# Kernel tuning notes

Measured on AMD Instinct MI355X. Metric: run time of the kernel, lower is better.

Reference implementation:

```python
import jax, jax.numpy as jnp
import numpy as np

H = 512          # size_half
K = 16           # n_segments
B = 8192         # batch
WIDTH = 1.0 / K  # spline bin width


def setup_inputs() -> dict:
    key = jax.random.key(0)
    ks = jax.random.split(key, 4)
    v_in = jax.random.uniform(ks[0], (B, 2 * H), dtype=jnp.float32)  # config in [0,1]
    log_density = jax.random.normal(ks[1], (B, 1), dtype=jnp.float32)
    W1 = jax.random.normal(ks[2], (H, H), dtype=jnp.float32) * (1.0 / np.sqrt(H))
    b1 = jnp.zeros((H,), dtype=jnp.float32)
    W2 = jax.random.normal(ks[3], (H, H * K), dtype=jnp.float32) * (1.0 / np.sqrt(H))
    b2 = jnp.zeros((H * K,), dtype=jnp.float32)
    return {"v_in": v_in, "log_density": log_density, "W1": W1, "b1": b1, "W2": W2, "b2": b2}


def reference(v_in, log_density, W1, b1, W2, b2):
    # even_sites=True: passive = first half, active = second half
    v_passive = v_in[:, :H]           # [B, H]
    v_active = v_in[:, H:]            # [B, H]

    # FullyConnectedNeuralNetwork: hidden layer + final layer, tanh activation on both
    h = jnp.tanh((v_passive - 0.5) @ W1 + b1)          # [B, H]
    net = jnp.tanh(h @ W2 + b2).reshape(-1, H, K)      # [B, H, K]
    p = jax.nn.softmax(net, axis=2)                    # bin probability masses P_k

    # y-coordinates of knots: CDF of the bin masses, with leading zero
    knots_y = jnp.concatenate(
        [jnp.zeros((p.shape[0], H, 1), p.dtype), jnp.cumsum(p, axis=2)], axis=2
    )                                                  # [B, H, K+1]

    # searchsorted on uniform knots linspace(0,1,K+1), then -1, clamped
    knots_x = jnp.linspace(0.0, 1.0, K + 1, dtype=v_in.dtype)
    k = jnp.clip(jnp.searchsorted(knots_x, v_active, side="left") - 1, 0, K - 1)  # [B, H]

    p_k = jnp.take_along_axis(p, k[..., None], axis=2)[..., 0]        # [B, H]
    y_lo = jnp.take_along_axis(knots_y, k[..., None], axis=2)[..., 0]  # [B, H]

    alpha = (v_active - k.astype(v_in.dtype) * WIDTH) / WIDTH          # [B, H]
    v_out_active = y_lo + alpha * p_k

    v_out = jnp.concatenate([v_passive, v_out_active], axis=1)         # [B, 2H]
    log_density_out = log_density - jnp.sum(jnp.log(p_k), axis=1, keepdims=True)  # [B, 1]
    return v_out, log_density_out
```

## Files before the change

kernel.cpp:

```cpp
#include <hip/hip_runtime.h>
#include <hip/hip_bf16.h>

#define HH   512
#define BB   8192
#define WIDTH (1.0f/16.0f)

typedef __attribute__((ext_vector_type(8))) short  short8;
typedef __attribute__((ext_vector_type(4))) float  floatx4;

typedef const __attribute__((address_space(1))) void* gptr_t;
typedef __attribute__((address_space(3))) void*       lptr_t;

__device__ __forceinline__ void gload_lds16(const void* g, void* l) {
    __builtin_amdgcn_global_load_lds((gptr_t)g, (lptr_t)l, 16, 0, 0);
}

__device__ __forceinline__ float tanh_fast(float x) {
    float e = __expf(2.0f * x);
    return 1.0f - 2.0f * __builtin_amdgcn_rcpf(e + 1.0f);
}

__global__ void prep_small(const float* __restrict__ vin, const float* __restrict__ W1,
                           const float* __restrict__ ld,
                           float* __restrict__ vout, float* __restrict__ ldout,
                           __hip_bfloat16* __restrict__ Abf,
                           __hip_bfloat16* __restrict__ W1T) {
    __shared__ __align__(16) float tile[32 * 36];
    int bid = blockIdx.x, tid = threadIdx.x;
    if (bid < 256) {
        int c0 = (bid & 15) * 32, r0 = (bid >> 4) * 32;
        int y  = tid >> 3;
        int x0 = (tid & 7) * 4;
        float4 v = *(const float4*)(W1 + (size_t)(r0 + y) * 512 + c0 + x0);
        *(float4*)(tile + y * 36 + x0) = v;
        __syncthreads();
        int n  = tid >> 3;
        int k4 = (tid & 7) * 4;
        union { __hip_bfloat16 h[4]; uint2 u; } o;
        o.h[0] = __float2bfloat16(tile[(k4 + 0) * 36 + n]);
        o.h[1] = __float2bfloat16(tile[(k4 + 1) * 36 + n]);
        o.h[2] = __float2bfloat16(tile[(k4 + 2) * 36 + n]);
        o.h[3] = __float2bfloat16(tile[(k4 + 3) * 36 + n]);
        *(uint2*)(W1T + (size_t)(c0 + n) * 512 + r0 + k4) = o.u;
    } else {
        int b = bid - 256;
        int i = b * 256 + tid;
        int r = i >> 6, c = i & 63;
        const float4* src = (const float4*)(vin + (size_t)r * 1024 + c * 8);
        float4 f0 = src[0], f1 = src[1];
        float4* dst = (float4*)(vout + (size_t)r * 1024 + c * 8);
        dst[0] = f0; dst[1] = f1;
        union { __hip_bfloat16 h[8]; uint4 v; } u;
        u.h[0] = __float2bfloat16(f0.x - 0.5f); u.h[1] = __float2bfloat16(f0.y - 0.5f);
        u.h[2] = __float2bfloat16(f0.z - 0.5f); u.h[3] = __float2bfloat16(f0.w - 0.5f);
        u.h[4] = __float2bfloat16(f1.x - 0.5f); u.h[5] = __float2bfloat16(f1.y - 0.5f);
        u.h[6] = __float2bfloat16(f1.z - 0.5f); u.h[7] = __float2bfloat16(f1.w - 0.5f);
        *(uint4*)(Abf + (size_t)r * 512 + c * 8) = u.v;
        if (tid < 4) { int row = b * 4 + tid; ldout[row] = ld[row]; }
    }
}

__global__ __launch_bounds__(256, 4) void mega1_kernel(
        const __hip_bfloat16* __restrict__ Abf,
        const __hip_bfloat16* __restrict__ W1T,
        const float* __restrict__ b1,
        __hip_bfloat16* __restrict__ hM,
        const float* __restrict__ W2,
        __hip_bfloat16* __restrict__ W2T) {
    __shared__ __align__(16) char smem[32768];
    int bid = blockIdx.x, tid = threadIdx.x;
    if (bid >= 256) {
        float* tile = (float*)smem;
        int b = bid - 256;
        int c0 = (b & 255) * 32, r0 = (b >> 8) * 32;
        int y  = tid >> 3;
        int x0 = (tid & 7) * 4;
        float4 v = *(const float4*)(W2 + (size_t)(r0 + y) * 8192 + c0 + x0);
        *(float4*)(tile + y * 36 + x0) = v;
        __syncthreads();
        int n  = tid >> 3;
        int k4 = (tid & 7) * 4;
        union { __hip_bfloat16 h[4]; uint2 u; } o;
        o.h[0] = __float2bfloat16(tile[(k4 + 0) * 36 + n]);
        o.h[1] = __float2bfloat16(tile[(k4 + 1) * 36 + n]);
        o.h[2] = __float2bfloat16(tile[(k4 + 2) * 36 + n]);
        o.h[3] = __float2bfloat16(tile[(k4 + 3) * 36 + n]);
        *(uint2*)(W2T + (size_t)(c0 + n) * 512 + r0 + k4) = o.u;
        return;
    }
    short* ldsA = (short*)smem;
    short* ldsB = (short*)(smem + 16384);
    int lane = tid & 63;
    int wv = tid >> 6, wr = wv >> 1, wc = wv & 1;
    int q = lane >> 4, cx = lane & 15;
    int srow = tid >> 3;
    int skw  = ((tid & 7) ^ (srow & 7)) * 8;
    int rowBase = (bid >> 2) * 128;
    int colBase = (bid & 3) * 128;
    floatx4 acc[4][4] = {};

    for (int k0 = 0; k0 < HH; k0 += 64) {
        #pragma unroll
        for (int j = 0; j < 4; ++j) {
            int row = j * 32 + srow;
            unsigned loff = __builtin_amdgcn_readfirstlane((unsigned)((j * 256 + (tid & 192)) * 16));
            gload_lds16(Abf + (size_t)(rowBase + row) * HH + k0 + skw, (char*)ldsA + loff);
            gload_lds16(W1T + (size_t)(colBase + row) * HH + k0 + skw, (char*)ldsB + loff);
        }
        __syncthreads();
        #pragma unroll
        for (int s = 0; s < 2; ++s) {
            short8 a[4], b[4];
            #pragma unroll
            for (int mt = 0; mt < 4; ++mt)
                a[mt] = *(const short8*)(ldsA + (wr * 64 + mt * 16 + cx) * 64
                                              + (((s * 4 + q) ^ (cx & 7)) << 3));
            #pragma unroll
            for (int nt = 0; nt < 4; ++nt)
                b[nt] = *(const short8*)(ldsB + (wc * 64 + nt * 16 + cx) * 64
                                              + (((s * 4 + q) ^ (cx & 7)) << 3));
            #pragma unroll
            for (int mt = 0; mt < 4; ++mt)
                #pragma unroll
                for (int nt = 0; nt < 4; ++nt)
                    acc[mt][nt] = __builtin_amdgcn_mfma_f32_16x16x32_bf16(a[mt], b[nt], acc[mt][nt], 0, 0, 0);
        }
        __syncthreads();
    }

    float b1v[4];
    #pragma unroll
    for (int nt = 0; nt < 4; ++nt) b1v[nt] = b1[colBase + wc * 64 + nt * 16 + cx];
    #pragma unroll
    for (int mt = 0; mt < 4; ++mt)
        #pragma unroll
        for (int nt = 0; nt < 4; ++nt) {
            int col = colBase + wc * 64 + nt * 16 + cx;
            #pragma unroll
            for (int r = 0; r < 4; ++r) {
                int row = rowBase + wr * 64 + mt * 16 + q * 4 + r;
                hM[(size_t)row * HH + col] = __float2bfloat16(tanh_fast(acc[mt][nt][r] + b1v[nt]));
            }
        }
}

__global__ __launch_bounds__(256, 4) void gemm2_kernel(
        const __hip_bfloat16* __restrict__ hM,
        const __hip_bfloat16* __restrict__ W2T,
        const float* __restrict__ b2,
        const float* __restrict__ vin,
        float* __restrict__ vout,
        float* __restrict__ ldout) {
    __shared__ __align__(16) char smem[32768];
    short* ldsA = (short*)smem;
    short* ldsB = (short*)(smem + 16384);
    float* ldsE = (float*)smem;
    int tid = threadIdx.x;
    int lane = tid & 63;
    int wv = tid >> 6, wr = wv >> 1, wc = wv & 1;
    int q = lane >> 4, cx = lane & 15;
    int srow = tid >> 3;
    int skw  = ((tid & 7) ^ (srow & 7)) * 8;
    int bid = blockIdx.x;
    int xcd = bid & 7, w = bid >> 3;
    int by  = xcd * 8 + (w & 7);
    int bx  = w >> 3;
    int rowBase = by * 128;
    int colBase = bx * 128;
    floatx4 acc[4][4] = {};

    for (int k0 = 0; k0 < HH; k0 += 64) {
        #pragma unroll
        for (int j = 0; j < 4; ++j) {
            int row = j * 32 + srow;
            unsigned loff = __builtin_amdgcn_readfirstlane((unsigned)((j * 256 + (tid & 192)) * 16));
            gload_lds16(hM  + (size_t)(rowBase + row) * HH + k0 + skw, (char*)ldsA + loff);
            gload_lds16(W2T + (size_t)(colBase + row) * HH + k0 + skw, (char*)ldsB + loff);
        }
        __syncthreads();
        #pragma unroll
        for (int s = 0; s < 2; ++s) {
            short8 a[4], b[4];
            #pragma unroll
            for (int mt = 0; mt < 4; ++mt)
                a[mt] = *(const short8*)(ldsA + (wr * 64 + mt * 16 + cx) * 64
                                              + (((s * 4 + q) ^ (cx & 7)) << 3));
            #pragma unroll
            for (int nt = 0; nt < 4; ++nt)
                b[nt] = *(const short8*)(ldsB + (wc * 64 + nt * 16 + cx) * 64
                                              + (((s * 4 + q) ^ (cx & 7)) << 3));
            #pragma unroll
            for (int mt = 0; mt < 4; ++mt)
                #pragma unroll
                for (int nt = 0; nt < 4; ++nt)
                    acc[mt][nt] = __builtin_amdgcn_mfma_f32_16x16x32_bf16(a[mt], b[nt], acc[mt][nt], 0, 0, 0);
        }
        __syncthreads();
    }

    float b2v[4];
    #pragma unroll
    for (int nt = 0; nt < 4; ++nt) b2v[nt] = b2[colBase + wc * 64 + nt * 16 + cx];

    float* myTile = ldsE + wv * (16 * 76);
    int rowL  = lane & 15;
    int gL    = lane >> 4;
    int gAbs  = bx * 8 + wc * 4 + gL;

    #pragma unroll
    for (int mt = 0; mt < 4; ++mt) {
        #pragma unroll
        for (int nt = 0; nt < 4; ++nt)
            #pragma unroll
            for (int r = 0; r < 4; ++r)
                myTile[(q * 4 + r) * 76 + nt * 16 + cx] = acc[mt][nt][r] + b2v[nt];

        floatx4 x0 = *(const floatx4*)(myTile + rowL * 76 + gL * 16);
        floatx4 x1 = *(const floatx4*)(myTile + rowL * 76 + gL * 16 + 4);
        floatx4 x2 = *(const floatx4*)(myTile + rowL * 76 + gL * 16 + 8);
        floatx4 x3 = *(const floatx4*)(myTile + rowL * 76 + gL * 16 + 12);
        float xs[16] = { x0[0],x0[1],x0[2],x0[3], x1[0],x1[1],x1[2],x1[3],
                         x2[0],x2[1],x2[2],x2[3], x3[0],x3[1],x3[2],x3[3] };

        int row = rowBase + wr * 64 + mt * 16 + rowL;
        float v = vin[(size_t)row * 1024 + 512 + gAbs];
        int k = (int)ceilf(v * 16.0f) - 1;
        k = min(15, max(0, k));

        float s = 0.0f, csum = 0.0f, ek = 0.0f;
        #pragma unroll
        for (int j = 0; j < 16; ++j) {
            float e2 = __expf(2.0f * xs[j]);
            float t  = 1.0f - 2.0f * __builtin_amdgcn_rcpf(e2 + 1.0f);
            float e  = __expf(t);
            csum += (j < k)  ? e : 0.0f;
            ek    = (j == k) ? e : ek;
            s += e;
        }
        float rs = __builtin_amdgcn_rcpf(s);
        float pk  = ek * rs;
        float ylo = csum * rs;
        float alpha = (v - (float)k * WIDTH) * 16.0f;
        vout[(size_t)row * 1024 + 512 + gAbs] = ylo + alpha * pk;

        float logp = __logf(pk);
        logp += __shfl_xor(logp, 16, 64);
        logp += __shfl_xor(logp, 32, 64);
        if (lane < 16) atomicAdd(ldout + row, -logp);
    }
}

extern "C" void kernel_launch(void* const* d_in, const int* in_sizes, int n_in,
                              void* d_out, int out_size, void* d_ws, size_t ws_size,
                              hipStream_t stream) {
    const float* vin = (const float*)d_in[0];
    const float* ld  = (const float*)d_in[1];
    const float* W1  = (const float*)d_in[2];
    const float* b1  = (const float*)d_in[3];
    const float* W2  = (const float*)d_in[4];
    const float* b2  = (const float*)d_in[5];
    float* vout  = (float*)d_out;
    float* ldout = vout + (size_t)BB * 1024;

    char* ws = (char*)d_ws;
    __hip_bfloat16* Abf = (__hip_bfloat16*)(ws);
    __hip_bfloat16* W1T = (__hip_bfloat16*)(ws + 8388608);
    __hip_bfloat16* W2T = (__hip_bfloat16*)(ws + 8912896);
    __hip_bfloat16* hM  = (__hip_bfloat16*)(ws + 17301504);

    prep_small<<<2304, 256, 0, stream>>>(vin, W1, ld, vout, ldout, Abf, W1T);
    mega1_kernel<<<4352, 256, 0, stream>>>(Abf, W1T, b1, hM, W2, W2T);
    gemm2_kernel<<<4096, 256, 0, stream>>>(hM, W2T, b2, vin, vout, ldout);
}
```

Baseline: 197.0 us.

## Fuse input/W1 bf16 conversion into GEMM1 and drop the prep kernel

```diff
diff --git a/kernel.cpp b/kernel.cpp
--- a/kernel.cpp
+++ b/kernel.cpp
@@ -20,55 +20,29 @@
     return 1.0f - 2.0f * __builtin_amdgcn_rcpf(e + 1.0f);
 }
 
-__global__ void prep_small(const float* __restrict__ vin, const float* __restrict__ W1,
-                           const float* __restrict__ ld,
-                           float* __restrict__ vout, float* __restrict__ ldout,
-                           __hip_bfloat16* __restrict__ Abf,
-                           __hip_bfloat16* __restrict__ W1T) {
-    __shared__ __align__(16) float tile[32 * 36];
+__global__ __launch_bounds__(256, 4) void mega_kernel(
+        const float* __restrict__ vin,
+        const float* __restrict__ W1,
+        const float* __restrict__ b1,
+        __hip_bfloat16* __restrict__ hM,
+        const float* __restrict__ W2,
+        __hip_bfloat16* __restrict__ W2T,
+        const float* __restrict__ ld,
+        float* __restrict__ vout, float* __restrict__ ldout) {
+    __shared__ __align__(16) char smem[32768];
     int bid = blockIdx.x, tid = threadIdx.x;
-    if (bid < 256) {
-        int c0 = (bid & 15) * 32, r0 = (bid >> 4) * 32;
-        int y  = tid >> 3;
-        int x0 = (tid & 7) * 4;
-        float4 v = *(const float4*)(W1 + (size_t)(r0 + y) * 512 + c0 + x0);
-        *(float4*)(tile + y * 36 + x0) = v;
-        __syncthreads();
-        int n  = tid >> 3;
-        int k4 = (tid & 7) * 4;
-        union { __hip_bfloat16 h[4]; uint2 u; } o;
-        o.h[0] = __float2bfloat16(tile[(k4 + 0) * 36 + n]);
-        o.h[1] = __float2bfloat16(tile[(k4 + 1) * 36 + n]);
-        o.h[2] = __float2bfloat16(tile[(k4 + 2) * 36 + n]);
-        o.h[3] = __float2bfloat16(tile[(k4 + 3) * 36 + n]);
-        *(uint2*)(W1T + (size_t)(c0 + n) * 512 + r0 + k4) = o.u;
-    } else {
-        int b = bid - 256;
+
+    if (bid >= 4352) {
+        int b = bid - 4352;
         int i = b * 256 + tid;
         int r = i >> 6, c = i & 63;
         const float4* src = (const float4*)(vin + (size_t)r * 1024 + c * 8);
         float4 f0 = src[0], f1 = src[1];
         float4* dst = (float4*)(vout + (size_t)r * 1024 + c * 8);
         dst[0] = f0; dst[1] = f1;
-        union { __hip_bfloat16 h[8]; uint4 v; } u;
-        u.h[0] = __float2bfloat16(f0.x - 0.5f); u.h[1] = __float2bfloat16(f0.y - 0.5f);
-        u.h[2] = __float2bfloat16(f0.z - 0.5f); u.h[3] = __float2bfloat16(f0.w - 0.5f);
-        u.h[4] = __float2bfloat16(f1.x - 0.5f); u.h[5] = __float2bfloat16(f1.y - 0.5f);
-        u.h[6] = __float2bfloat16(f1.z - 0.5f); u.h[7] = __float2bfloat16(f1.w - 0.5f);
-        *(uint4*)(Abf + (size_t)r * 512 + c * 8) = u.v;
         if (tid < 4) { int row = b * 4 + tid; ldout[row] = ld[row]; }
-    }
-}
-
-__global__ __launch_bounds__(256, 4) void mega1_kernel(
-        const __hip_bfloat16* __restrict__ Abf,
-        const __hip_bfloat16* __restrict__ W1T,
-        const float* __restrict__ b1,
-        __hip_bfloat16* __restrict__ hM,
-        const float* __restrict__ W2,
-        __hip_bfloat16* __restrict__ W2T) {
-    __shared__ __align__(16) char smem[32768];
-    int bid = blockIdx.x, tid = threadIdx.x;
+        return;
+    }
     if (bid >= 256) {
         float* tile = (float*)smem;
         int b = bid - 256;
@@ -88,37 +62,72 @@
         *(uint2*)(W2T + (size_t)(c0 + n) * 512 + r0 + k4) = o.u;
         return;
     }
+
     short* ldsA = (short*)smem;
     short* ldsB = (short*)(smem + 16384);
     int lane = tid & 63;
     int wv = tid >> 6, wr = wv >> 1, wc = wv & 1;
     int q = lane >> 4, cx = lane & 15;
-    int srow = tid >> 3;
-    int skw  = ((tid & 7) ^ (srow & 7)) * 8;
     int rowBase = (bid >> 2) * 128;
     int colBase = (bid & 3) * 128;
+    int ar = tid >> 1;
+    int ah = tid & 1;
+    int cb = tid & 31;
+    int kb0 = tid >> 5;
+    const float* aSrc = vin + (size_t)(rowBase + ar) * 1024 + ah * 32;
     floatx4 acc[4][4] = {};
 
     for (int k0 = 0; k0 < HH; k0 += 64) {
         #pragma unroll
-        for (int j = 0; j < 4; ++j) {
-            int row = j * 32 + srow;
-            unsigned loff = __builtin_amdgcn_readfirstlane((unsigned)((j * 256 + (tid & 192)) * 16));
-            gload_lds16(Abf + (size_t)(rowBase + row) * HH + k0 + skw, (char*)ldsA + loff);
-            gload_lds16(W1T + (size_t)(colBase + row) * HH + k0 + skw, (char*)ldsB + loff);
+        for (int i = 0; i < 4; ++i) {
+            float4 f0 = *(const float4*)(aSrc + k0 + i * 8);
+            float4 f1 = *(const float4*)(aSrc + k0 + i * 8 + 4);
+            union { __hip_bfloat16 h[8]; short8 v; } u;
+            u.h[0] = __float2bfloat16(f0.x - 0.5f); u.h[1] = __float2bfloat16(f0.y - 0.5f);
+            u.h[2] = __float2bfloat16(f0.z - 0.5f); u.h[3] = __float2bfloat16(f0.w - 0.5f);
+            u.h[4] = __float2bfloat16(f1.x - 0.5f); u.h[5] = __float2bfloat16(f1.y - 0.5f);
+            u.h[6] = __float2bfloat16(f1.z - 0.5f); u.h[7] = __float2bfloat16(f1.w - 0.5f);
+            int kc = ah * 4 + i;
+            *(short8*)(ldsA + ar * 64 + ((kc ^ (ar & 7)) << 3)) = u.v;
+        }
+        #pragma unroll
+        for (int bb = 0; bb < 2; ++bb) {
+            int kb = kb0 + bb * 8;
+            const float* bSrc = W1 + (size_t)(k0 + kb * 4) * 512 + colBase + cb * 4;
+            float4 r0 = *(const float4*)(bSrc);
+            float4 r1 = *(const float4*)(bSrc + 512);
+            float4 r2 = *(const float4*)(bSrc + 1024);
+            float4 r3 = *(const float4*)(bSrc + 1536);
+            int kc = kb >> 1, kh = (kb & 1) * 4;
+            union { __hip_bfloat16 h[4]; uint2 u; } o;
+            #pragma unroll
+            for (int cc = 0; cc < 4; ++cc) {
+                float v0 = (cc == 0) ? r0.x : (cc == 1) ? r0.y : (cc == 2) ? r0.z : r0.w;
+                float v1 = (cc == 0) ? r1.x : (cc == 1) ? r1.y : (cc == 2) ? r1.z : r1.w;
+                float v2 = (cc == 0) ? r2.x : (cc == 1) ? r2.y : (cc == 2) ? r2.z : r2.w;
+                float v3 = (cc == 0) ? r3.x : (cc == 1) ? r3.y : (cc == 2) ? r3.z : r3.w;
+                o.h[0] = __float2bfloat16(v0); o.h[1] = __float2bfloat16(v1);
+                o.h[2] = __float2bfloat16(v2); o.h[3] = __float2bfloat16(v3);
+                int col = cb * 4 + cc;
+                int gr  = kc ^ ((col & 7) ^ ((col >> 2) & 7));
+                *(uint2*)(ldsB + col * 64 + (gr << 3) + kh) = o.u;
+            }
         }
         __syncthreads();
         #pragma unroll
         for (int s = 0; s < 2; ++s) {
             short8 a[4], b[4];
             #pragma unroll
-            for (int mt = 0; mt < 4; ++mt)
-                a[mt] = *(const short8*)(ldsA + (wr * 64 + mt * 16 + cx) * 64
-                                              + (((s * 4 + q) ^ (cx & 7)) << 3));
-            #pragma unroll
-            for (int nt = 0; nt < 4; ++nt)
-                b[nt] = *(const short8*)(ldsB + (wc * 64 + nt * 16 + cx) * 64
-                                              + (((s * 4 + q) ^ (cx & 7)) << 3));
+            for (int mt = 0; mt < 4; ++mt) {
+                int row = wr * 64 + mt * 16 + cx;
+                a[mt] = *(const short8*)(ldsA + row * 64 + (((s * 4 + q) ^ (row & 7)) << 3));
+            }
+            #pragma unroll
+            for (int nt = 0; nt < 4; ++nt) {
+                int row = wc * 64 + nt * 16 + cx;
+                int sw  = (row & 7) ^ ((row >> 2) & 7);
+                b[nt] = *(const short8*)(ldsB + row * 64 + (((s * 4 + q) ^ sw) << 3));
+            }
             #pragma unroll
             for (int mt = 0; mt < 4; ++mt)
                 #pragma unroll
@@ -263,12 +272,9 @@
     float* ldout = vout + (size_t)BB * 1024;
 
     char* ws = (char*)d_ws;
-    __hip_bfloat16* Abf = (__hip_bfloat16*)(ws);
-    __hip_bfloat16* W1T = (__hip_bfloat16*)(ws + 8388608);
-    __hip_bfloat16* W2T = (__hip_bfloat16*)(ws + 8912896);
-    __hip_bfloat16* hM  = (__hip_bfloat16*)(ws + 17301504);
-
-    prep_small<<<2304, 256, 0, stream>>>(vin, W1, ld, vout, ldout, Abf, W1T);
-    mega1_kernel<<<4352, 256, 0, stream>>>(Abf, W1T, b1, hM, W2, W2T);
+    __hip_bfloat16* W2T = (__hip_bfloat16*)(ws);
+    __hip_bfloat16* hM  = (__hip_bfloat16*)(ws + 8388608);
+
+    mega_kernel<<<6400, 256, 0, stream>>>(vin, W1, b1, hM, W2, W2T, ld, vout, ldout);
     gemm2_kernel<<<4096, 256, 0, stream>>>(hM, W2T, b2, vin, vout, ldout);
 }
```

New measurement: 215.3 us. 1.09x slower.
